# Optimization experiments

Measured on AMD Instinct MI355X. Metric: run time of the kernel, lower is better.

## Reference

```python
import jax, jax.numpy as jnp
import numpy as np
import math

B, S = 2, 2048                      # batch, seq_len (equal-length varlen pack)
NUM_HEADS, HEAD_DIM = 32, 128
NUM_KV_HEADS = 8                    # GQA group size = 4
WINDOW = 1024                       # sliding window (window_size, 0)
SCALE = 1.0 / math.sqrt(HEAD_DIM)


def get_slopes(n):
    # n=32 is a power of two -> simple geometric slopes (matches torch get_slopes)
    start = 2.0 ** (-2.0 ** (-(math.log2(n) - 3)))
    return np.array([start * start ** i for i in range(n)], dtype=np.float32)


def setup_inputs() -> dict:
    key = jax.random.key(0)
    kq, kk, kv = jax.random.split(key, 3)
    q = jax.random.normal(kq, (B * S, NUM_HEADS * HEAD_DIM), dtype=jnp.float32)
    k = jax.random.normal(kk, (B * S, NUM_KV_HEADS * HEAD_DIM), dtype=jnp.float32)
    v = jax.random.normal(kv, (B * S, NUM_KV_HEADS * HEAD_DIM), dtype=jnp.float32)
    return {"q": q, "k": k, "v": v}


def reference(q, k, v):
    # Prefill self-attention path of Attention.forward:
    # flash_attn_varlen_func(q, k, v, causal=True, window_size=(WINDOW, 0),
    #                        alibi_slopes=get_slopes(num_heads), softmax_scale=SCALE)
    slopes = jnp.asarray(get_slopes(NUM_HEADS))               # [H]
    qh = q.reshape(B, S, NUM_HEADS, HEAD_DIM)                 # [B,S,H,D]
    g = NUM_HEADS // NUM_KV_HEADS
    kh = jnp.repeat(k.reshape(B, S, NUM_KV_HEADS, HEAD_DIM), g, axis=2)
    vh = jnp.repeat(v.reshape(B, S, NUM_KV_HEADS, HEAD_DIM), g, axis=2)

    scores = jnp.einsum('bihd,bjhd->bhij', qh, kh) * SCALE    # [B,H,S,S]
    i = jnp.arange(S)[:, None]
    j = jnp.arange(S)[None, :]
    mask = (j <= i) & (j >= i - WINDOW)                       # causal + sliding window
    alibi = -slopes[:, None, None] * (i - j).astype(jnp.float32)  # [H,S,S]
    neg_inf = jnp.asarray(-jnp.inf, dtype=scores.dtype)
    scores = jnp.where(mask[None, None], scores + alibi[None], neg_inf)
    p = jax.nn.softmax(scores, axis=-1)
    o = jnp.einsum('bhij,bjhd->bihd', p, vh)                  # [B,S,H,D]
    return o.reshape(B * S, NUM_HEADS * HEAD_DIM)
```

## Files before the change

### kernel.cpp

```cpp
#include <hip/hip_runtime.h>
#include <stdint.h>

#define NB 2
#define NS 2048
#define NH 32
#define NKV 8
#define ND 128
#define NWIN 1024
#define KVB 32
#define SCALE2 (0.08838834764831845f * 1.4426950408889634f)
#define LOG2E 1.4426950408889634f

typedef __bf16 bf16x8 __attribute__((ext_vector_type(8)));
typedef float f32x4 __attribute__((ext_vector_type(4)));
typedef unsigned short u16x4 __attribute__((ext_vector_type(4)));
typedef unsigned short u16x8 __attribute__((ext_vector_type(8)));
typedef unsigned int u32x2 __attribute__((ext_vector_type(2)));

union Frag { u16x8 u; bf16x8 b; u32x2 w[2]; __bf16 e[8]; };
union BF4 { u16x4 u; __bf16 b[4]; };
union BF8 { u16x8 u; __bf16 b[8]; };

__device__ __forceinline__ void gload16(const unsigned short* g, unsigned short* l) {
  __builtin_amdgcn_global_load_lds(
      (const __attribute__((address_space(1))) unsigned int*)g,
      (__attribute__((address_space(3))) unsigned int*)l, 16, 0, 0);
}

__global__ __launch_bounds__(256)
void cvt_kv(const float* __restrict__ k, const float* __restrict__ v,
            unsigned short* __restrict__ kbf, unsigned short* __restrict__ vbf) {
  const int i = blockIdx.x * blockDim.x + threadIdx.x;
  float4 a0 = ((const float4*)k)[i * 2], a1 = ((const float4*)k)[i * 2 + 1];
  float4 b0 = ((const float4*)v)[i * 2], b1 = ((const float4*)v)[i * 2 + 1];
  BF8 ko, vo;
  ko.b[0] = (__bf16)a0.x; ko.b[1] = (__bf16)a0.y; ko.b[2] = (__bf16)a0.z; ko.b[3] = (__bf16)a0.w;
  ko.b[4] = (__bf16)a1.x; ko.b[5] = (__bf16)a1.y; ko.b[6] = (__bf16)a1.z; ko.b[7] = (__bf16)a1.w;
  vo.b[0] = (__bf16)b0.x; vo.b[1] = (__bf16)b0.y; vo.b[2] = (__bf16)b0.z; vo.b[3] = (__bf16)b0.w;
  vo.b[4] = (__bf16)b1.x; vo.b[5] = (__bf16)b1.y; vo.b[6] = (__bf16)b1.z; vo.b[7] = (__bf16)b1.w;
  ((u16x8*)kbf)[i] = ko.u;
  ((u16x8*)vbf)[i] = vo.u;
}

__global__ __launch_bounds__(256, 2)
void attn_gqa(const unsigned short* __restrict__ kbf,
              const unsigned short* __restrict__ vbf,
              const float* __restrict__ qg, float* __restrict__ og) {
  __shared__ unsigned short k_lds[2][KVB * 128];
  __shared__ unsigned short v_lds[2][KVB * 128];

  const int tid = threadIdx.x;
  const int w = tid >> 6;
  const int lane = tid & 63;
  const int l15 = lane & 15;
  const int lg = lane >> 4;

  const int bid = blockIdx.x;
  const int hkv = bid & 7;
  const int rest = bid >> 3;
  const int b = (rest >= 48) ? 1 : 0;
  const int slot = rest - b * 48;
  const int h = hkv * 4 + w;
  const float slope2 = exp2f(-0.25f * (float)(h + 1)) * LOG2E;

  int koff_e[2], voff_e[2];
#pragma unroll
  for (int i = 0; i < 2; ++i) {
    const int rk = (w * 2 + i) * 4 + lg;
    const int c = l15;
    const int sig = ((rk >> 2) & 3) * 8 + ((rk >> 4) & 1) * 4 + (rk & 3);
    koff_e[i] = sig * (NKV * ND) + ((c ^ (rk & 7)) * 8);
    const int e0 = (w * 2 + i) * 512 + lane * 8;
    const int sx0 = e0 & 15;
    const int vj = (e0 >> 4) & 3;
    const int vg_ = (e0 >> 6) & 3;
    const int s1 = (e0 >> 8) & 1;
    const int scv = (e0 >> 9) & 7;
    voff_e[i] = (vg_ * 8 + s1 * 4 + vj) * (NKV * ND) + scv * 16 + sx0;
  }
  const unsigned short* kpan = kbf + (size_t)b * NS * (NKV * ND) + hkv * ND;
  const unsigned short* vpan = vbf + (size_t)b * NS * (NKV * ND) + hkv * ND;

  auto stage = [&](int t, int buf) {
    const size_t eb = (size_t)(t * KVB) * (NKV * ND);
#pragma unroll
    for (int i = 0; i < 2; ++i) {
      gload16(kpan + eb + koff_e[i], &k_lds[buf][(w * 2 + i) * 512]);
      gload16(vpan + eb + voff_e[i], &v_lds[buf][(w * 2 + i) * 512]);
    }
  };

  auto run_band = [&](int q0) {
    const int qiA = q0 + l15;
    const int qiB = qiA + 16;

    u16x8 qfA[4], qfB[4];
#pragma unroll
    for (int half = 0; half < 2; ++half) {
      const int qi = half ? qiB : qiA;
      const float* qp = qg + (size_t)(b * NS + qi) * (NH * ND) + h * ND;
#pragma unroll
      for (int ks = 0; ks < 4; ++ks) {
        const int dbase = ks * 32 + lg * 8;
        float4 f0 = *(const float4*)(qp + dbase);
        float4 f1 = *(const float4*)(qp + dbase + 4);
        Frag q_;
        q_.e[0] = (__bf16)f0.x; q_.e[1] = (__bf16)f0.y;
        q_.e[2] = (__bf16)f0.z; q_.e[3] = (__bf16)f0.w;
        q_.e[4] = (__bf16)f1.x; q_.e[5] = (__bf16)f1.y;
        q_.e[6] = (__bf16)f1.z; q_.e[7] = (__bf16)f1.w;
        if (half) qfB[ks] = q_.u; else qfA[ks] = q_.u;
      }
    }

    float mA = -1e30f, lA = 0.f, mB = -1e30f, lB = 0.f;
    f32x4 accA[8], accB[8];
#pragma unroll
    for (int c = 0; c < 8; ++c) {
      accA[c][0] = 0.f; accA[c][1] = 0.f; accA[c][2] = 0.f; accA[c][3] = 0.f;
      accB[c][0] = 0.f; accB[c][1] = 0.f; accB[c][2] = 0.f; accB[c][3] = 0.f;
    }

    const int t0 = (q0 >= NWIN) ? ((q0 - NWIN) >> 5) : 0;
    const int t1 = q0 >> 5;

    int cur = 0;
    stage(t0, 0);

    for (int t = t0; t <= t1; ++t) {
      const int kvbase = t * KVB;
      if (t < t1) {
        stage(t + 1, cur ^ 1);
        asm volatile("s_waitcnt vmcnt(4)" ::: "memory");
      } else {
        asm volatile("s_waitcnt vmcnt(0)" ::: "memory");
      }
      __builtin_amdgcn_s_barrier();

      const bool interior = (kvbase + 31 <= q0) && (kvbase >= q0 + 31 - NWIN);

      f32x4 sA[2], sB[2];
#pragma unroll
      for (int f = 0; f < 2; ++f) {
        sA[f][0] = 0.f; sA[f][1] = 0.f; sA[f][2] = 0.f; sA[f][3] = 0.f;
        sB[f][0] = 0.f; sB[f][1] = 0.f; sB[f][2] = 0.f; sB[f][3] = 0.f;
      }
      const int xo = (l15 & 7) << 4;
#pragma unroll
      for (int ks = 0; ks < 4; ++ks) {
        const int db2 = ks * 64 + lg * 16;
        Frag qa, qb;
        qa.u = qfA[ks]; qb.u = qfB[ks];
#pragma unroll
        for (int f = 0; f < 2; ++f) {
          Frag kb;
          kb.u = *(const u16x8*)((const char*)&k_lds[cur][0] +
                                 (((f * 16 + l15) * 256 + db2) ^ xo));
          sA[f] = __builtin_amdgcn_mfma_f32_16x16x32_bf16(kb.b, qa.b, sA[f], 0, 0, 0);
          sB[f] = __builtin_amdgcn_mfma_f32_16x16x32_bf16(kb.b, qb.b, sB[f], 0, 0, 0);
        }
      }

      Frag pbA, pbB;
      auto softmax_half = [&](const f32x4* s, int dbse, float& m_r, float& l_r,
                              f32x4* acc, Frag& pb) {
        float sv[2][4];
        if (interior) {
          const float abase = -slope2 * (float)dbse;
#pragma unroll
          for (int f = 0; f < 2; ++f)
#pragma unroll
            for (int r = 0; r < 4; ++r)
              sv[f][r] = fmaf(s[f][r], SCALE2,
                              fmaf(slope2, (float)(f * 4 + r), abase));
        } else {
#pragma unroll
          for (int f = 0; f < 2; ++f)
#pragma unroll
            for (int r = 0; r < 4; ++r) {
              const int d = dbse - (f * 4 + r);
              const float val = fmaf(s[f][r], SCALE2, -slope2 * (float)d);
              sv[f][r] = ((unsigned)d <= (unsigned)NWIN) ? val : -1e30f;
            }
        }
        float tm = fmaxf(fmaxf(sv[0][0], sv[0][1]), fmaxf(sv[0][2], sv[0][3]));
        tm = fmaxf(tm, fmaxf(fmaxf(sv[1][0], sv[1][1]), fmaxf(sv[1][2], sv[1][3])));
        tm = fmaxf(tm, __shfl_xor(tm, 16, 64));
        tm = fmaxf(tm, __shfl_xor(tm, 32, 64));
        if (!__all(tm <= m_r + 8.0f)) {
          const float newm = fmaxf(m_r, tm);
          const float fac = __builtin_amdgcn_exp2f(m_r - newm);
          m_r = newm;
          l_r *= fac;
#pragma unroll
          for (int c = 0; c < 8; ++c) acc[c] = acc[c] * fac;
        }
        float rs = 0.f;
#pragma unroll
        for (int f = 0; f < 2; ++f) {
          float e0 = __builtin_amdgcn_exp2f(sv[f][0] - m_r);
          float e1 = __builtin_amdgcn_exp2f(sv[f][1] - m_r);
          float e2 = __builtin_amdgcn_exp2f(sv[f][2] - m_r);
          float e3 = __builtin_amdgcn_exp2f(sv[f][3] - m_r);
          rs += (e0 + e1) + (e2 + e3);
          pb.e[f * 4 + 0] = (__bf16)e0; pb.e[f * 4 + 1] = (__bf16)e1;
          pb.e[f * 4 + 2] = (__bf16)e2; pb.e[f * 4 + 3] = (__bf16)e3;
        }
        rs += __shfl_xor(rs, 16, 64);
        rs += __shfl_xor(rs, 32, 64);
        l_r += rs;
      };
      softmax_half(sA, qiA - kvbase - lg * 8, mA, lA, accA, pbA);
      softmax_half(sB, qiB - kvbase - lg * 8, mB, lB, accB, pbB);

      const unsigned int vbase = (unsigned int)(uintptr_t)(&v_lds[cur][0]) + lane * 8;
#pragma unroll
      for (int c = 0; c < 8; ++c) {
        u32x2 r0, r1;
        const unsigned int a = vbase + c * 1024;
        asm volatile("ds_read_b64_tr_b16 %0, %1" : "=v"(r0) : "v"(a));
        asm volatile("ds_read_b64_tr_b16 %0, %1 offset:512" : "=v"(r1) : "v"(a));
        asm volatile("s_waitcnt lgkmcnt(0)" ::: "memory");
        __builtin_amdgcn_sched_barrier(0);
        Frag vb;
        vb.w[0] = r0; vb.w[1] = r1;
        accA[c] = __builtin_amdgcn_mfma_f32_16x16x32_bf16(vb.b, pbA.b, accA[c], 0, 0, 0);
        accB[c] = __builtin_amdgcn_mfma_f32_16x16x32_bf16(vb.b, pbB.b, accB[c], 0, 0, 0);
      }
      __builtin_amdgcn_sched_barrier(0);
      __builtin_amdgcn_s_barrier();
      cur ^= 1;
    }

    {
      const float inv = 1.0f / lA;
      float* op = og + (size_t)(b * NS + qiA) * (NH * ND) + h * ND + lg * 4;
#pragma unroll
      for (int c = 0; c < 8; ++c) { f32x4 o = accA[c] * inv; *(f32x4*)(op + c * 16) = o; }
    }
    {
      const float inv = 1.0f / lB;
      float* op = og + (size_t)(b * NS + qiB) * (NH * ND) + h * ND + lg * 4;
#pragma unroll
      for (int c = 0; c < 8; ++c) { f32x4 o = accB[c] * inv; *(f32x4*)(op + c * 16) = o; }
    }
  };

  if (slot < 32) {
    run_band((slot + 32) * 32);
  } else {
    const int s = slot - 32;
    run_band(s * 32);
    run_band((31 - s) * 32);
  }
}

__global__ __launch_bounds__(256, 2)
void attn_fb(const float* __restrict__ qg, const float* __restrict__ kg,
             const float* __restrict__ vg, float* __restrict__ og) {
  __shared__ unsigned short k_lds[64 * 128];
  __shared__ unsigned short v_lds[64 * 128];
  const int tid = threadIdx.x;
  const int w = tid >> 6;
  const int lane = tid & 63;
  const int l15 = lane & 15;
  const int lg = lane >> 4;
  const int bid = blockIdx.x;
  const int h = bid & 31;
  const int qt = 31 - ((bid >> 5) & 31);
  const int b = bid >> 10;
  const int hkv = h >> 2;
  const float slope2 = exp2f(-0.25f * (float)(h + 1)) * LOG2E;
  const int q0 = qt * 64;
  const int qi = q0 + w * 16 + l15;
  u16x8 qf[4];
  {
    const float* qp = qg + (size_t)(b * NS + qi) * (NH * ND) + h * ND;
#pragma unroll
    for (int ks = 0; ks < 4; ++ks) {
      const int dbase = ks * 32 + lg * 8;
      float4 f0 = *(const float4*)(qp + dbase);
      float4 f1 = *(const float4*)(qp + dbase + 4);
      Frag q_;
      q_.e[0] = (__bf16)f0.x; q_.e[1] = (__bf16)f0.y;
      q_.e[2] = (__bf16)f0.z; q_.e[3] = (__bf16)f0.w;
      q_.e[4] = (__bf16)f1.x; q_.e[5] = (__bf16)f1.y;
      q_.e[6] = (__bf16)f1.z; q_.e[7] = (__bf16)f1.w;
      qf[ks] = q_.u;
    }
  }
  float m_r = -1e30f, l_r = 0.f;
  f32x4 acc[8];
#pragma unroll
  for (int c = 0; c < 8; ++c) { acc[c][0] = 0.f; acc[c][1] = 0.f; acc[c][2] = 0.f; acc[c][3] = 0.f; }
  const int srow = tid >> 5;
  const int sdb = (tid & 31) * 4;
  const int sc = sdb >> 4;
  const int sx = sdb & 15;
  float4 kreg[8], vreg[8];
  const int t0 = (q0 >= NWIN) ? ((q0 - NWIN) >> 6) : 0;
  const int t1 = q0 >> 6;
  auto load_tile = [&](int t) {
    const int kvbase = t * 64;
#pragma unroll
    for (int it = 0; it < 8; ++it) {
      const size_t go = (size_t)(b * NS + kvbase + it * 8 + srow) * (NKV * ND) + hkv * ND + sdb;
      kreg[it] = *(const float4*)(kg + go);
      vreg[it] = *(const float4*)(vg + go);
    }
  };
  load_tile(t0);
  for (int t = t0; t <= t1; ++t) {
    const int kvbase = t * 64;
    __syncthreads();
#pragma unroll
    for (int it = 0; it < 8; ++it) {
      const int row = it * 8 + srow;
      BF4 ku, vu;
      ku.b[0] = (__bf16)kreg[it].x; ku.b[1] = (__bf16)kreg[it].y;
      ku.b[2] = (__bf16)kreg[it].z; ku.b[3] = (__bf16)kreg[it].w;
      vu.b[0] = (__bf16)vreg[it].x; vu.b[1] = (__bf16)vreg[it].y;
      vu.b[2] = (__bf16)vreg[it].z; vu.b[3] = (__bf16)vreg[it].w;
      const int rk = ((row & 4) << 3) | ((row & 56) >> 1) | (row & 3);
      const int kb = (rk * 256 + sdb * 2) ^ ((rk & 7) << 4);
      *(u16x4*)((char*)k_lds + kb) = ku.u;
      const int s2 = ((row >> 5) << 1) | ((row >> 2) & 1);
      const int vi = sc * 1024 + s2 * 256 + ((row >> 3) & 3) * 64 + (row & 3) * 16 + sx;
      *(u16x4*)(&v_lds[vi]) = vu.u;
    }
    __syncthreads();
    if (t < t1) load_tile(t + 1);
    f32x4 s[4];
#pragma unroll
    for (int f = 0; f < 4; ++f) { s[f][0] = 0.f; s[f][1] = 0.f; s[f][2] = 0.f; s[f][3] = 0.f; }
    const int xo = (l15 & 7) << 4;
#pragma unroll
    for (int ks = 0; ks < 4; ++ks) {
      const int db2 = ks * 64 + lg * 16;
      Frag qa; qa.u = qf[ks];
#pragma unroll
      for (int f = 0; f < 4; ++f) {
        Frag kb;
        kb.u = *(u16x8*)((char*)k_lds + (((f * 16 + l15) * 256 + db2) ^ xo));
        s[f] = __builtin_amdgcn_mfma_f32_16x16x32_bf16(kb.b, qa.b, s[f], 0, 0, 0);
      }
    }
    const int dbse = qi - kvbase - lg * 8;
    float sv[4][4];
#pragma unroll
    for (int f = 0; f < 4; ++f) {
#pragma unroll
      for (int r = 0; r < 4; ++r) {
        const int koff = ((f & 1) << 5) + ((f >> 1) << 2) + r;
        const int d = dbse - koff;
        const float val = fmaf(s[f][r], SCALE2, -slope2 * (float)d);
        sv[f][r] = ((unsigned)d <= (unsigned)NWIN) ? val : -1e30f;
      }
    }
    float tm = fmaxf(fmaxf(sv[0][0], sv[0][1]), fmaxf(sv[0][2], sv[0][3]));
#pragma unroll
    for (int f = 1; f < 4; ++f)
      tm = fmaxf(tm, fmaxf(fmaxf(sv[f][0], sv[f][1]), fmaxf(sv[f][2], sv[f][3])));
    tm = fmaxf(tm, __shfl_xor(tm, 16, 64));
    tm = fmaxf(tm, __shfl_xor(tm, 32, 64));
    const float newm = fmaxf(m_r, tm);
    const float fac = __builtin_amdgcn_exp2f(m_r - newm);
    m_r = newm;
    float rs = 0.f;
    Frag pb0, pb1;
#pragma unroll
    for (int f = 0; f < 4; ++f) {
      float e0 = __builtin_amdgcn_exp2f(sv[f][0] - m_r);
      float e1 = __builtin_amdgcn_exp2f(sv[f][1] - m_r);
      float e2 = __builtin_amdgcn_exp2f(sv[f][2] - m_r);
      float e3 = __builtin_amdgcn_exp2f(sv[f][3] - m_r);
      rs += (e0 + e1) + (e2 + e3);
      const int base = (f >> 1) * 4;
      if (f & 1) {
        pb1.e[base + 0] = (__bf16)e0; pb1.e[base + 1] = (__bf16)e1;
        pb1.e[base + 2] = (__bf16)e2; pb1.e[base + 3] = (__bf16)e3;
      } else {
        pb0.e[base + 0] = (__bf16)e0; pb0.e[base + 1] = (__bf16)e1;
        pb0.e[base + 2] = (__bf16)e2; pb0.e[base + 3] = (__bf16)e3;
      }
    }
    rs += __shfl_xor(rs, 16, 64);
    rs += __shfl_xor(rs, 32, 64);
    l_r = l_r * fac + rs;
#pragma unroll
    for (int c = 0; c < 8; ++c) acc[c] = acc[c] * fac;
    const unsigned int vbase = (unsigned int)(uintptr_t)(&v_lds[0]) + lane * 8;
#pragma unroll
    for (int c = 0; c < 8; ++c) {
      u32x2 r0, r1, r2, r3;
      const unsigned int a = vbase + c * 2048;
      asm volatile("ds_read_b64_tr_b16 %0, %1" : "=v"(r0) : "v"(a));
      asm volatile("ds_read_b64_tr_b16 %0, %1 offset:512" : "=v"(r1) : "v"(a));
      asm volatile("ds_read_b64_tr_b16 %0, %1 offset:1024" : "=v"(r2) : "v"(a));
      asm volatile("ds_read_b64_tr_b16 %0, %1 offset:1536" : "=v"(r3) : "v"(a));
      asm volatile("s_waitcnt lgkmcnt(0)" ::: "memory");
      __builtin_amdgcn_sched_barrier(0);
      Frag vb0, vb1;
      vb0.w[0] = r0; vb0.w[1] = r1;
      vb1.w[0] = r2; vb1.w[1] = r3;
      acc[c] = __builtin_amdgcn_mfma_f32_16x16x32_bf16(vb0.b, pb0.b, acc[c], 0, 0, 0);
      acc[c] = __builtin_amdgcn_mfma_f32_16x16x32_bf16(vb1.b, pb1.b, acc[c], 0, 0, 0);
    }
  }
  const float inv = 1.0f / l_r;
  float* op = og + (size_t)(b * NS + qi) * (NH * ND) + h * ND + lg * 4;
#pragma unroll
  for (int c = 0; c < 8; ++c) { f32x4 o = acc[c] * inv; *(f32x4*)(op + c * 16) = o; }
}

extern "C" void kernel_launch(void* const* d_in, const int* in_sizes, int n_in,
                              void* d_out, int out_size, void* d_ws, size_t ws_size,
                              hipStream_t stream) {
  (void)in_sizes; (void)n_in; (void)out_size;
  const float* q = (const float*)d_in[0];
  const float* k = (const float*)d_in[1];
  const float* v = (const float*)d_in[2];
  float* out = (float*)d_out;
  const size_t kv_elems = (size_t)NB * NS * NKV * ND;
  const size_t need = 2 * kv_elems * sizeof(unsigned short);
  if (ws_size >= need) {
    unsigned short* kbf = (unsigned short*)d_ws;
    unsigned short* vbf = kbf + kv_elems;
    cvt_kv<<<dim3((unsigned)(kv_elems / 8 / 256)), dim3(256), 0, stream>>>(k, v, kbf, vbf);
    attn_gqa<<<dim3(NB * NKV * 48), dim3(256), 0, stream>>>(kbf, vbf, q, out);
  } else {
    attn_fb<<<dim3(NB * NH * (NS / 64)), dim3(256), 0, stream>>>(q, k, v, out);
  }
}
```

Measured before the change: 135.5 us.

## Reverse KV tile order, defer row-sum reductions, and software-pipeline V LDS reads

Walks the KV tiles from the diagonal backwards, so the running max is usually set by the first tile and rescaling is rarely needed. The cross-lane shuffles for the row max now run only when a rescale is triggered. The row-sum shuffles are deferred to the end of the loop. V transposed LDS reads are prefetched four fragments ahead, with graded lgkmcnt waits instead of a full wait before each MFMA. MFMA sections get raised wave priority, and the launch bound drops its min-blocks hint, which may change register allocation and occupancy.

```diff
diff --git a/kernel.cpp b/kernel.cpp
--- a/kernel.cpp
+++ b/kernel.cpp
@@ -42,7 +42,7 @@
   ((u16x8*)vbf)[i] = vo.u;
 }
 
-__global__ __launch_bounds__(256, 2)
+__global__ __launch_bounds__(256)
 void attn_gqa(const unsigned short* __restrict__ kbf,
               const unsigned short* __restrict__ vbf,
               const float* __restrict__ qg, float* __restrict__ og) {
@@ -125,12 +125,12 @@
     const int t1 = q0 >> 5;
 
     int cur = 0;
-    stage(t0, 0);
-
-    for (int t = t0; t <= t1; ++t) {
+    stage(t1, 0);
+
+    for (int t = t1; t >= t0; --t) {
       const int kvbase = t * KVB;
-      if (t < t1) {
-        stage(t + 1, cur ^ 1);
+      if (t > t0) {
+        stage(t - 1, cur ^ 1);
         asm volatile("s_waitcnt vmcnt(4)" ::: "memory");
       } else {
         asm volatile("s_waitcnt vmcnt(0)" ::: "memory");
@@ -146,6 +146,7 @@
         sB[f][0] = 0.f; sB[f][1] = 0.f; sB[f][2] = 0.f; sB[f][3] = 0.f;
       }
       const int xo = (l15 & 7) << 4;
+      __builtin_amdgcn_s_setprio(1);
 #pragma unroll
       for (int ks = 0; ks < 4; ++ks) {
         const int db2 = ks * 64 + lg * 16;
@@ -160,6 +161,7 @@
           sB[f] = __builtin_amdgcn_mfma_f32_16x16x32_bf16(kb.b, qb.b, sB[f], 0, 0, 0);
         }
       }
+      __builtin_amdgcn_s_setprio(0);
 
       Frag pbA, pbB;
       auto softmax_half = [&](const f32x4* s, int dbse, float& m_r, float& l_r,
@@ -185,9 +187,9 @@
         }
         float tm = fmaxf(fmaxf(sv[0][0], sv[0][1]), fmaxf(sv[0][2], sv[0][3]));
         tm = fmaxf(tm, fmaxf(fmaxf(sv[1][0], sv[1][1]), fmaxf(sv[1][2], sv[1][3])));
-        tm = fmaxf(tm, __shfl_xor(tm, 16, 64));
-        tm = fmaxf(tm, __shfl_xor(tm, 32, 64));
         if (!__all(tm <= m_r + 8.0f)) {
+          tm = fmaxf(tm, __shfl_xor(tm, 16, 64));
+          tm = fmaxf(tm, __shfl_xor(tm, 32, 64));
           const float newm = fmaxf(m_r, tm);
           const float fac = __builtin_amdgcn_exp2f(m_r - newm);
           m_r = newm;
@@ -206,32 +208,45 @@
           pb.e[f * 4 + 0] = (__bf16)e0; pb.e[f * 4 + 1] = (__bf16)e1;
           pb.e[f * 4 + 2] = (__bf16)e2; pb.e[f * 4 + 3] = (__bf16)e3;
         }
-        rs += __shfl_xor(rs, 16, 64);
-        rs += __shfl_xor(rs, 32, 64);
         l_r += rs;
       };
       softmax_half(sA, qiA - kvbase - lg * 8, mA, lA, accA, pbA);
       softmax_half(sB, qiB - kvbase - lg * 8, mB, lB, accB, pbB);
 
+      Frag vb4[4];
       const unsigned int vbase = (unsigned int)(uintptr_t)(&v_lds[cur][0]) + lane * 8;
 #pragma unroll
+      for (int cp = 0; cp < 4; ++cp) {
+        const unsigned int a = vbase + cp * 1024;
+        asm volatile("ds_read_b64_tr_b16 %0, %1" : "=v"(vb4[cp].w[0]) : "v"(a));
+        asm volatile("ds_read_b64_tr_b16 %0, %1 offset:512" : "=v"(vb4[cp].w[1]) : "v"(a));
+      }
+      __builtin_amdgcn_s_setprio(1);
+#pragma unroll
       for (int c = 0; c < 8; ++c) {
-        u32x2 r0, r1;
-        const unsigned int a = vbase + c * 1024;
-        asm volatile("ds_read_b64_tr_b16 %0, %1" : "=v"(r0) : "v"(a));
-        asm volatile("ds_read_b64_tr_b16 %0, %1 offset:512" : "=v"(r1) : "v"(a));
-        asm volatile("s_waitcnt lgkmcnt(0)" ::: "memory");
+        if (c == 5)      asm volatile("s_waitcnt lgkmcnt(4)" ::: "memory");
+        else if (c == 6) asm volatile("s_waitcnt lgkmcnt(2)" ::: "memory");
+        else if (c == 7) asm volatile("s_waitcnt lgkmcnt(0)" ::: "memory");
+        else             asm volatile("s_waitcnt lgkmcnt(6)" ::: "memory");
         __builtin_amdgcn_sched_barrier(0);
-        Frag vb;
-        vb.w[0] = r0; vb.w[1] = r1;
-        accA[c] = __builtin_amdgcn_mfma_f32_16x16x32_bf16(vb.b, pbA.b, accA[c], 0, 0, 0);
-        accB[c] = __builtin_amdgcn_mfma_f32_16x16x32_bf16(vb.b, pbB.b, accB[c], 0, 0, 0);
-      }
+        accA[c] = __builtin_amdgcn_mfma_f32_16x16x32_bf16(vb4[c & 3].b, pbA.b, accA[c], 0, 0, 0);
+        accB[c] = __builtin_amdgcn_mfma_f32_16x16x32_bf16(vb4[c & 3].b, pbB.b, accB[c], 0, 0, 0);
+        if (c < 4) {
+          const unsigned int a2 = vbase + (c + 4) * 1024;
+          asm volatile("ds_read_b64_tr_b16 %0, %1" : "=v"(vb4[c].w[0]) : "v"(a2));
+          asm volatile("ds_read_b64_tr_b16 %0, %1 offset:512" : "=v"(vb4[c].w[1]) : "v"(a2));
+        }
+      }
+      __builtin_amdgcn_s_setprio(0);
       __builtin_amdgcn_sched_barrier(0);
       __builtin_amdgcn_s_barrier();
       cur ^= 1;
     }
 
+    lA += __shfl_xor(lA, 16, 64);
+    lA += __shfl_xor(lA, 32, 64);
+    lB += __shfl_xor(lB, 16, 64);
+    lB += __shfl_xor(lB, 32, 64);
     {
       const float inv = 1.0f / lA;
       float* op = og + (size_t)(b * NS + qiA) * (NH * ND) + h * ND + lg * 4;
```

After: 122.0 us. -9.9%, faster.
